# Optimization experiments

Hardware: AMD Instinct MI355X
Metric: run time of the kernel (lower is better)

## Reference

```python
import jax, jax.numpy as jnp
import numpy as np
from jax.ops import segment_sum, segment_max

N, E, IN_DIM, HID, HEADS, B, ACTIONS = 16384, 262144, 512, 256, 4, 64, 32
NEG_SLOPE = 0.2  # PyG GATConv default leaky-relu slope


def setup_inputs() -> dict:
    key = jax.random.key(0)
    ks = jax.random.split(key, 12)
    x = jax.random.normal(ks[0], (N, IN_DIM), dtype=jnp.float32)
    edge_index = jax.random.randint(ks[1], (2, E), 0, N, dtype=jnp.int64)
    batch = jnp.sort(jax.random.randint(ks[2], (N,), 0, B, dtype=jnp.int64))
    s = 0.05
    return {
        "x": x,
        "edge_index": edge_index,
        "batch": batch,
        # SAGEConv: lin_l (neighbors, with bias) + lin_r (root, no bias)
        "sage_w_l": jax.random.normal(ks[3], (IN_DIM, HID), dtype=jnp.float32) * s,
        "sage_b_l": jnp.zeros((HID,), dtype=jnp.float32),
        "sage_w_r": jax.random.normal(ks[4], (IN_DIM, HID), dtype=jnp.float32) * s,
        # GATConv: shared lin, per-head attention vectors, output bias (concat=False)
        "gat_w": jax.random.normal(ks[5], (HID, HEADS * HID), dtype=jnp.float32) * s,
        "gat_att_src": jax.random.normal(ks[6], (HEADS, HID), dtype=jnp.float32) * s,
        "gat_att_dst": jax.random.normal(ks[7], (HEADS, HID), dtype=jnp.float32) * s,
        "gat_b": jnp.zeros((HID,), dtype=jnp.float32),
        # action head
        "head_w": jax.random.normal(ks[8], (HID, ACTIONS), dtype=jnp.float32) * s,
        "head_b": jnp.zeros((ACTIONS,), dtype=jnp.float32),
    }


def reference(x, edge_index, batch, sage_w_l, sage_b_l, sage_w_r,
              gat_w, gat_att_src, gat_att_dst, gat_b, head_w, head_b):
    src, dst = edge_index[0], edge_index[1]

    # ---- SAGEConv (mean aggregation): lin_l(mean_j x_j) + lin_r(x_i) ----
    agg = segment_sum(x[src], dst, num_segments=N)                 # [N, IN_DIM]
    deg = segment_sum(jnp.ones((E,), x.dtype), dst, num_segments=N)
    mean_nbr = agg / jnp.maximum(deg, 1.0)[:, None]
    h = mean_nbr @ sage_w_l + sage_b_l + x @ sage_w_r              # [N, HID]
    h = jax.nn.relu(h)
    # dropout is identity at inference (training=False)

    # ---- GATConv (adds self-loops, concat=False -> head average) ----
    loop = jnp.arange(N, dtype=src.dtype)
    si = jnp.concatenate([src, loop])                              # [E2]
    di = jnp.concatenate([dst, loop])
    g = (h @ gat_w).reshape(N, HEADS, HID)                         # [N, H, C]
    a_src = jnp.einsum('nhc,hc->nh', g, gat_att_src)               # [N, H]
    a_dst = jnp.einsum('nhc,hc->nh', g, gat_att_dst)
    logits = jax.nn.leaky_relu(a_src[si] + a_dst[di], NEG_SLOPE)   # [E2, H]
    m = segment_max(logits, di, num_segments=N)                    # per-target max
    ex = jnp.exp(logits - m[di])
    denom = segment_sum(ex, di, num_segments=N)
    alpha = ex / denom[di]                                         # [E2, H]
    out = segment_sum(g[si] * alpha[:, :, None], di, num_segments=N)  # [N, H, C]
    out = jax.nn.relu(out.mean(axis=1) + gat_b)                    # [N, HID]

    # ---- global mean pool + action head ----
    pooled = segment_sum(out, batch, num_segments=B)
    cnt = segment_sum(jnp.ones((N,), out.dtype), batch, num_segments=B)
    pooled = pooled / jnp.maximum(cnt, 1.0)[:, None]               # [B, HID]
    return pooled @ head_w + head_b                                # [B, ACTIONS]
```

## Files before the change

kernel.cpp:

```cpp
#include <hip/hip_runtime.h>
#include <math.h>

#define N_NODES 16384
#define N_EDGES 262144
#define IN_DIM  512
#define HID     256
#define HEADS   4
#define NBATCH  64
#define ACTIONS 32
#define NEG_SLOPE 0.2f

typedef __attribute__((ext_vector_type(8))) short short8;
typedef __attribute__((ext_vector_type(4))) float f32x4;

__device__ __forceinline__ float lrelu(float v) { return v > 0.f ? v : NEG_SLOPE * v; }

__device__ __forceinline__ unsigned short bf16_rne(float f) {
    union { float f; unsigned int u; } x; x.f = f;
    unsigned int u = x.u;
    unsigned int r = (u + 0x7FFFu + ((u >> 16) & 1u)) >> 16;
    return (unsigned short)r;
}

__device__ __forceinline__ float bf16_to_f32(unsigned short s) {
    union { unsigned int u; float f; } x; x.u = (unsigned int)s << 16;
    return x.f;
}

__device__ __forceinline__ float4 bf4_to_f4(ushort4 u) {
    return make_float4(bf16_to_f32(u.x), bf16_to_f32(u.y), bf16_to_f32(u.z), bf16_to_f32(u.w));
}

__device__ __forceinline__ void async_copy16(const unsigned short* g, unsigned short* l) {
    __builtin_amdgcn_global_load_lds(
        (const __attribute__((address_space(1))) unsigned int*)g,
        (__attribute__((address_space(3))) unsigned int*)l, 16, 0, 0);
}

#define NB_WLR  1024
#define NB_WSTK 1024
#define NB_WATT 8
#define NB_ZERO 128
#define NB_SETUP (NB_WLR + NB_WSTK + NB_WATT + NB_ZERO)

__global__ __launch_bounds__(256) void setup_kernel(
        const float* __restrict__ wl, const float* __restrict__ wr, unsigned short* __restrict__ bt1,
        const float* __restrict__ gat_w, unsigned short* __restrict__ bt2,
        const float* __restrict__ att_src, const float* __restrict__ att_dst, float* __restrict__ watt,
        int* __restrict__ deg, float* __restrict__ pooled) {
    int bid = blockIdx.x, tid = threadIdx.x;
    if (bid < NB_WLR) {
        int idx = bid * 256 + tid;
        int j = idx >> 9;
        int k = idx & 511;
        float v = (j < HID) ? wl[k * HID + j] : wr[k * HID + (j - HID)];
        bt1[idx] = bf16_rne(v);
    } else if (bid < NB_WLR + NB_WSTK) {
        int idx = (bid - NB_WLR) * 256 + tid;
        int c = idx >> 10;
        int r = idx & 1023;
        int h = r >> 8;
        int k = r & 255;
        bt2[idx] = bf16_rne(gat_w[(size_t)k * (HEADS * HID) + h * HID + c]);
    } else if (bid < NB_WLR + NB_WSTK + NB_WATT) {
        int j = bid - NB_WLR - NB_WSTK;
        int c = tid;
        int hh = j & 3;
        const float* att = (j < 4) ? (att_src + hh * HID) : (att_dst + hh * HID);
        float s = 0.f;
        for (int cc = 0; cc < HID; cc++)
            s += gat_w[(size_t)c * (HEADS * HID) + hh * HID + cc] * att[cc];
        watt[j * HID + c] = s;
    } else {
        int idx = (bid - NB_WLR - NB_WSTK - NB_WATT) * 256 + tid;
        if (idx < N_NODES) deg[idx] = 0;
        else pooled[idx - N_NODES] = 0.f;
    }
}

__global__ void deg_kernel(const int* __restrict__ ei, int* __restrict__ deg) {
    int e = blockIdx.x * 256 + threadIdx.x;
    if (e < N_EDGES) atomicAdd(&deg[ei[N_EDGES + e]], 1);
}

__global__ __launch_bounds__(256) void scan_kernel(const int* __restrict__ deg,
                                                   int* __restrict__ row_start,
                                                   int* __restrict__ pos) {
    int t = threadIdx.x;
    int lane = t & 63, wv = t >> 6;
    int base = t * 64;
    int4 buf[16];
    int sum = 0;
#pragma unroll
    for (int i = 0; i < 16; i++) {
        buf[i] = ((const int4*)(deg + base))[i];
        sum += buf[i].x + buf[i].y + buf[i].z + buf[i].w;
    }
    int v = sum;
#pragma unroll
    for (int off = 1; off < 64; off <<= 1) {
        int u = __shfl_up(v, off);
        if (lane >= off) v += u;
    }
    __shared__ int wsum[4];
    if (lane == 63) wsum[wv] = v;
    __syncthreads();
    int wbase = 0;
    for (int w0 = 0; w0 < wv; w0++) wbase += wsum[w0];
    int run = wbase + v - sum;
#pragma unroll
    for (int i = 0; i < 16; i++) {
        int4 b = buf[i];
        int4 o;
        o.x = run; run += b.x;
        o.y = run; run += b.y;
        o.z = run; run += b.z;
        o.w = run; run += b.w;
        ((int4*)(row_start + base))[i] = o;
        ((int4*)(pos + base))[i] = o;
    }
    if (t == 255) row_start[N_NODES] = run;
}

__global__ void fill_kernel(const int* __restrict__ ei, int* __restrict__ pos,
                            int* __restrict__ col) {
    int e = blockIdx.x * 256 + threadIdx.x;
    if (e < N_EDGES) {
        int s = ei[e];
        int d = ei[N_EDGES + e];
        int p = atomicAdd(&pos[d], 1);
        col[p] = s;
    }
}

#define BK 32

__global__ __launch_bounds__(256) void gemm1_kernel(const float* __restrict__ X,
                                                    const unsigned short* __restrict__ Bt,
                                                    unsigned short* __restrict__ Cb,
                                                    int Nn, int K) {
    __shared__ __align__(16) unsigned short As[2][64 * BK];
    __shared__ __align__(16) unsigned short Bs[2][128 * BK];

    int tid  = threadIdx.x;
    int wv   = tid >> 6;
    int lane = tid & 63;
    int m0 = blockIdx.y * 64;
    int n0 = blockIdx.x * 128;
    int wm = (wv & 1) * 32;
    int wn = (wv >> 1) * 64;

    int srow = tid >> 2;
    int scol = (tid & 3) * 8;
    const float*          Xg  = X  + (size_t)(m0 + srow) * K + scol;
    const unsigned short* Bg0 = Bt + (size_t)(n0 + srow) * K + scol;
    const unsigned short* Bg1 = Bt + (size_t)(n0 + 64 + srow) * K + scol;

    int fr = lane & 15;
    int fk = (lane >> 4) * 8;
    f32x4 acc[2][4] = {};

    for (int kt = 0; kt < K; kt += 2 * BK) {
#pragma unroll
        for (int s = 0; s < 2; s++) {
            int ko = kt + s * BK;
            async_copy16(Bg0 + ko, &Bs[s][wv * 512]);
            async_copy16(Bg1 + ko, &Bs[s][2048 + wv * 512]);
            float4 a0 = *(const float4*)(Xg + ko);
            float4 a1 = *(const float4*)(Xg + ko + 4);
            short8 p;
            p[0] = (short)bf16_rne(a0.x); p[1] = (short)bf16_rne(a0.y);
            p[2] = (short)bf16_rne(a0.z); p[3] = (short)bf16_rne(a0.w);
            p[4] = (short)bf16_rne(a1.x); p[5] = (short)bf16_rne(a1.y);
            p[6] = (short)bf16_rne(a1.z); p[7] = (short)bf16_rne(a1.w);
            *(short8*)&As[s][srow * BK + scol] = p;
        }
        __syncthreads();

#pragma unroll
        for (int s = 0; s < 2; s++) {
            short8 af[2], bf[4];
#pragma unroll
            for (int mi = 0; mi < 2; mi++)
                af[mi] = *(const short8*)&As[s][(wm + mi * 16 + fr) * BK + fk];
#pragma unroll
            for (int ni = 0; ni < 4; ni++)
                bf[ni] = *(const short8*)&Bs[s][(wn + ni * 16 + fr) * BK + fk];
#pragma unroll
            for (int mi = 0; mi < 2; mi++)
#pragma unroll
                for (int ni = 0; ni < 4; ni++)
                    acc[mi][ni] = __builtin_amdgcn_mfma_f32_16x16x32_bf16(af[mi], bf[ni], acc[mi][ni], 0, 0, 0);
        }
        __syncthreads();
    }

    int cr = (lane >> 4) * 4;
    int cc = lane & 15;
#pragma unroll
    for (int mi = 0; mi < 2; mi++) {
#pragma unroll
        for (int ni = 0; ni < 4; ni++) {
            int gc = n0 + wn + ni * 16 + cc;
#pragma unroll
            for (int r = 0; r < 4; r++) {
                int gr = m0 + wm + mi * 16 + cr + r;
                Cb[(size_t)gr * Nn + gc] = bf16_rne(acc[mi][ni][r]);
            }
        }
    }
}

__global__ __launch_bounds__(256) void gemm2_pool_kernel(const unsigned short* __restrict__ A,
                                                         const unsigned short* __restrict__ Bt,
                                                         const int* __restrict__ batch,
                                                         const float* __restrict__ bias,
                                                         float scale,
                                                         float* __restrict__ pooled,
                                                         int Nn, int K) {
    __shared__ __align__(16) unsigned short As[2][64 * BK];
    __shared__ __align__(16) unsigned short Bs[2][64 * BK];
    __shared__ int bsh[64];

    int tid  = threadIdx.x;
    int wv   = tid >> 6;
    int lane = tid & 63;
    int m0 = blockIdx.y * 64;
    int n0 = blockIdx.x * 64;
    int wm = (wv & 1) * 32;
    int wn = (wv >> 1) * 32;

    if (tid < 64) bsh[tid] = batch[m0 + tid];

    int srow = tid >> 2;
    int scol = (tid & 3) * 8;
    const unsigned short* Ag = A  + (size_t)(m0 + srow) * K + scol;
    const unsigned short* Bg = Bt + (size_t)(n0 + srow) * K + scol;

    int fr = lane & 15;
    int fk = (lane >> 4) * 8;
    f32x4 acc[2][2] = {};

    for (int kt = 0; kt < K; kt += 2 * BK) {
#pragma unroll
        for (int s = 0; s < 2; s++) {
            int ko = kt + s * BK;
            async_copy16(Ag + ko, &As[s][wv * 512]);
            async_copy16(Bg + ko, &Bs[s][wv * 512]);
        }
        __syncthreads();

#pragma unroll
        for (int s = 0; s < 2; s++) {
            short8 af[2], bf[2];
#pragma unroll
            for (int mi = 0; mi < 2; mi++)
                af[mi] = *(const short8*)&As[s][(wm + mi * 16 + fr) * BK + fk];
#pragma unroll
            for (int ni = 0; ni < 2; ni++)
                bf[ni] = *(const short8*)&Bs[s][(wn + ni * 16 + fr) * BK + fk];
#pragma unroll
            for (int mi = 0; mi < 2; mi++)
#pragma unroll
                for (int ni = 0; ni < 2; ni++)
                    acc[mi][ni] = __builtin_amdgcn_mfma_f32_16x16x32_bf16(af[mi], bf[ni], acc[mi][ni], 0, 0, 0);
        }
        __syncthreads();
    }

    int cr = (lane >> 4) * 4;
    int cc = lane & 15;
#pragma unroll
    for (int mi = 0; mi < 2; mi++) {
        int rowb = wm + mi * 16 + cr;
        int b0 = bsh[rowb], b3 = bsh[rowb + 3];
#pragma unroll
        for (int ni = 0; ni < 2; ni++) {
            int gc = n0 + wn + ni * 16 + cc;
            float b = bias[gc];
            float v0 = fmaxf(fmaf(acc[mi][ni][0], scale, b), 0.f);
            float v1 = fmaxf(fmaf(acc[mi][ni][1], scale, b), 0.f);
            float v2 = fmaxf(fmaf(acc[mi][ni][2], scale, b), 0.f);
            float v3 = fmaxf(fmaf(acc[mi][ni][3], scale, b), 0.f);
            if (b0 == b3) {
                atomicAdd(&pooled[b0 * HID + gc], (v0 + v1) + (v2 + v3));
            } else {
                atomicAdd(&pooled[bsh[rowb + 0] * HID + gc], v0);
                atomicAdd(&pooled[bsh[rowb + 1] * HID + gc], v1);
                atomicAdd(&pooled[bsh[rowb + 2] * HID + gc], v2);
                atomicAdd(&pooled[bsh[rowb + 3] * HID + gc], v3);
            }
        }
    }
}

__global__ __launch_bounds__(256) void sage_agg_kernel(const unsigned short* __restrict__ xlr,
                                                       const int* __restrict__ row_start,
                                                       const int* __restrict__ col,
                                                       const float* __restrict__ b_l,
                                                       const float* __restrict__ watt,
                                                       unsigned short* __restrict__ hb,
                                                       float* __restrict__ a_att) {
    __shared__ float watt_s[8 * HID];
    for (int i = threadIdx.x; i < 8 * HID; i += 256) watt_s[i] = watt[i];
    __syncthreads();

    int wave = threadIdx.x >> 6;
    int lane = threadIdx.x & 63;
    int n = blockIdx.x * 4 + wave;
    int start = row_start[n], end = row_start[n + 1];
    int c0 = lane * 4;

    float4 acc = make_float4(0.f, 0.f, 0.f, 0.f);
    int e = start;
    for (; e + 4 <= end; e += 4) {
        int s0 = col[e], s1 = col[e + 1], s2 = col[e + 2], s3 = col[e + 3];
        ushort4 u0 = *(const ushort4*)(xlr + (size_t)s0 * IN_DIM + c0);
        ushort4 u1 = *(const ushort4*)(xlr + (size_t)s1 * IN_DIM + c0);
        ushort4 u2 = *(const ushort4*)(xlr + (size_t)s2 * IN_DIM + c0);
        ushort4 u3 = *(const ushort4*)(xlr + (size_t)s3 * IN_DIM + c0);
        float4 v0 = bf4_to_f4(u0), v1 = bf4_to_f4(u1), v2 = bf4_to_f4(u2), v3 = bf4_to_f4(u3);
        acc.x += (v0.x + v1.x) + (v2.x + v3.x);
        acc.y += (v0.y + v1.y) + (v2.y + v3.y);
        acc.z += (v0.z + v1.z) + (v2.z + v3.z);
        acc.w += (v0.w + v1.w) + (v2.w + v3.w);
    }
    for (; e < end; e++) {
        int s = col[e];
        float4 v = bf4_to_f4(*(const ushort4*)(xlr + (size_t)s * IN_DIM + c0));
        acc.x += v.x; acc.y += v.y; acc.z += v.z; acc.w += v.w;
    }
    float inv = 1.f / (float)max(end - start, 1);
    float4 xr = bf4_to_f4(*(const ushort4*)(xlr + (size_t)n * IN_DIM + HID + c0));
    float4 bl = *(const float4*)(b_l + c0);
    float4 hv;
    hv.x = fmaxf(fmaf(acc.x, inv, bl.x + xr.x), 0.f);
    hv.y = fmaxf(fmaf(acc.y, inv, bl.y + xr.y), 0.f);
    hv.z = fmaxf(fmaf(acc.z, inv, bl.z + xr.z), 0.f);
    hv.w = fmaxf(fmaf(acc.w, inv, bl.w + xr.w), 0.f);
    ushort4 ho;
    ho.x = bf16_rne(hv.x); ho.y = bf16_rne(hv.y); ho.z = bf16_rne(hv.z); ho.w = bf16_rne(hv.w);
    *(ushort4*)(hb + (size_t)n * HID + c0) = ho;

    float p[8];
#pragma unroll
    for (int j = 0; j < 8; j++) {
        float4 wt = *(const float4*)&watt_s[j * HID + c0];
        p[j] = hv.x * wt.x + hv.y * wt.y + hv.z * wt.z + hv.w * wt.w;
    }
#pragma unroll
    for (int off = 32; off; off >>= 1)
#pragma unroll
        for (int j = 0; j < 8; j++) p[j] += __shfl_down(p[j], off);
    if (lane == 0) {
#pragma unroll
        for (int j = 0; j < 8; j++) a_att[n * 8 + j] = p[j];
    }
}

__global__ __launch_bounds__(256) void gat_agg_kernel(const unsigned short* __restrict__ hb,
                                                      const float* __restrict__ a_att,
                                                      const int* __restrict__ row_start,
                                                      const int* __restrict__ col,
                                                      unsigned short* __restrict__ T) {
    __shared__ __align__(16) float w_s[4][64 * 4];
    int wave = threadIdx.x >> 6;
    int lane = threadIdx.x & 63;
    int n = blockIdx.x * 4 + wave;
    int start = row_start[n], end = row_start[n + 1];

    float4 an = *(const float4*)(a_att + n * 8);
    float4 ad = *(const float4*)(a_att + n * 8 + 4);
    float adst[4] = {ad.x, ad.y, ad.z, ad.w};
    float selfl[4] = {lrelu(an.x + ad.x), lrelu(an.y + ad.y), lrelu(an.z + ad.z), lrelu(an.w + ad.w)};
    float m[4], wself[4];
#pragma unroll
    for (int hh = 0; hh < 4; hh++) {
        m[hh] = fmaxf(selfl[hh], 0.f);
        wself[hh] = __expf(selfl[hh] - m[hh]);
    }

    int c0 = lane * 4;
    float4 hn = bf4_to_f4(*(const ushort4*)(hb + (size_t)n * HID + c0));
    float4 acc[4];
#pragma unroll
    for (int hh = 0; hh < 4; hh++)
        acc[hh] = make_float4(wself[hh] * hn.x, wself[hh] * hn.y, wself[hh] * hn.z, wself[hh] * hn.w);

    float dpart[4] = {0.f, 0.f, 0.f, 0.f};

    for (int base = start; base < end; base += 64) {
        int cnt = min(64, end - base);
        if (lane < cnt) {
            int s = col[base + lane];
            float4 as = *(const float4*)(a_att + s * 8);
            float4 wv;
            wv.x = __expf(lrelu(as.x + adst[0]) - m[0]);
            wv.y = __expf(lrelu(as.y + adst[1]) - m[1]);
            wv.z = __expf(lrelu(as.z + adst[2]) - m[2]);
            wv.w = __expf(lrelu(as.w + adst[3]) - m[3]);
            *(float4*)&w_s[wave][lane * 4] = wv;
            dpart[0] += wv.x; dpart[1] += wv.y; dpart[2] += wv.z; dpart[3] += wv.w;
        }
        __builtin_amdgcn_wave_barrier();

        int i = 0;
        for (; i + 2 <= cnt; i += 2) {
            int s0 = col[base + i], s1 = col[base + i + 1];
            float4 w0 = *(const float4*)&w_s[wave][i * 4];
            float4 w1 = *(const float4*)&w_s[wave][(i + 1) * 4];
            ushort4 u0 = *(const ushort4*)(hb + (size_t)s0 * HID + c0);
            ushort4 u1 = *(const ushort4*)(hb + (size_t)s1 * HID + c0);
            float4 h0 = bf4_to_f4(u0), h1 = bf4_to_f4(u1);
            float wr0[4] = {w0.x, w0.y, w0.z, w0.w};
            float wr1[4] = {w1.x, w1.y, w1.z, w1.w};
#pragma unroll
            for (int hh = 0; hh < 4; hh++) {
                acc[hh].x = fmaf(wr0[hh], h0.x, fmaf(wr1[hh], h1.x, acc[hh].x));
                acc[hh].y = fmaf(wr0[hh], h0.y, fmaf(wr1[hh], h1.y, acc[hh].y));
                acc[hh].z = fmaf(wr0[hh], h0.z, fmaf(wr1[hh], h1.z, acc[hh].z));
                acc[hh].w = fmaf(wr0[hh], h0.w, fmaf(wr1[hh], h1.w, acc[hh].w));
            }
        }
        if (i < cnt) {
            int s0 = col[base + i];
            float4 w0 = *(const float4*)&w_s[wave][i * 4];
            float4 h0 = bf4_to_f4(*(const ushort4*)(hb + (size_t)s0 * HID + c0));
            float wr0[4] = {w0.x, w0.y, w0.z, w0.w};
#pragma unroll
            for (int hh = 0; hh < 4; hh++) {
                acc[hh].x = fmaf(wr0[hh], h0.x, acc[hh].x);
                acc[hh].y = fmaf(wr0[hh], h0.y, acc[hh].y);
                acc[hh].z = fmaf(wr0[hh], h0.z, acc[hh].z);
                acc[hh].w = fmaf(wr0[hh], h0.w, acc[hh].w);
            }
        }
        __builtin_amdgcn_wave_barrier();
    }

#pragma unroll
    for (int off = 32; off; off >>= 1)
#pragma unroll
        for (int hh = 0; hh < 4; hh++) dpart[hh] += __shfl_down(dpart[hh], off);
    float invd[4];
#pragma unroll
    for (int hh = 0; hh < 4; hh++)
        invd[hh] = 1.f / (__shfl(dpart[hh], 0) + wself[hh]);

#pragma unroll
    for (int hh = 0; hh < 4; hh++) {
        ushort4 o;
        o.x = bf16_rne(acc[hh].x * invd[hh]); o.y = bf16_rne(acc[hh].y * invd[hh]);
        o.z = bf16_rne(acc[hh].z * invd[hh]); o.w = bf16_rne(acc[hh].w * invd[hh]);
        *(ushort4*)(T + (size_t)n * (HEADS * HID) + hh * HID + c0) = o;
    }
}

__device__ __forceinline__ int lower_bound_i(const int* a, int n, int v) {
    int lo = 0, hi = n;
    while (lo < hi) {
        int mid = (lo + hi) >> 1;
        if (a[mid] < v) lo = mid + 1; else hi = mid;
    }
    return lo;
}

__global__ __launch_bounds__(256) void head_kernel(const float* __restrict__ pooled,
                                                   const int* __restrict__ batch,
                                                   const float* __restrict__ head_w,
                                                   const float* __restrict__ head_b,
                                                   float* __restrict__ out) {
    __shared__ float sm[HID];
    int b = blockIdx.x;
    int c = threadIdx.x;
    int lo = lower_bound_i(batch, N_NODES, b);
    int hi = lower_bound_i(batch, N_NODES, b + 1);
    int cnt = hi - lo;
    sm[c] = pooled[b * HID + c] / (float)max(cnt, 1);
    __syncthreads();
    if (c < ACTIONS) {
        float acc = head_b[c];
        for (int k = 0; k < HID; k++) acc = fmaf(sm[k], head_w[k * ACTIONS + c], acc);
        out[b * ACTIONS + c] = acc;
    }
}

extern "C" void kernel_launch(void* const* d_in, const int* in_sizes, int n_in,
                              void* d_out, int out_size, void* d_ws, size_t ws_size,
                              hipStream_t stream) {
    const float* x        = (const float*)d_in[0];
    const int*   ei       = (const int*)d_in[1];
    const int*   batch    = (const int*)d_in[2];
    const float* sage_w_l = (const float*)d_in[3];
    const float* sage_b_l = (const float*)d_in[4];
    const float* sage_w_r = (const float*)d_in[5];
    const float* gat_w    = (const float*)d_in[6];
    const float* att_src  = (const float*)d_in[7];
    const float* att_dst  = (const float*)d_in[8];
    const float* gat_b    = (const float*)d_in[9];
    const float* head_w   = (const float*)d_in[10];
    const float* head_b   = (const float*)d_in[11];
    float* out = (float*)d_out;

    char* w = (char*)d_ws;
    float* a_att  = (float*)w; w += (size_t)N_NODES * 8 * 4;
    float* watt   = (float*)w; w += (size_t)8 * HID * 4;
    float* pooled = (float*)w; w += (size_t)NBATCH * HID * 4;
    unsigned short* xlr = (unsigned short*)w; w += (size_t)N_NODES * IN_DIM * 2;
    unsigned short* hb  = (unsigned short*)w; w += (size_t)N_NODES * HID * 2;
    unsigned short* T   = (unsigned short*)w; w += (size_t)N_NODES * HEADS * HID * 2;
    unsigned short* bt1 = (unsigned short*)w; w += (size_t)(2 * HID) * IN_DIM * 2;
    unsigned short* bt2 = (unsigned short*)w; w += (size_t)HID * (HEADS * HID) * 2;
    int* deg      = (int*)w;   w += (size_t)N_NODES * 4;
    int* row_start= (int*)w;   w += (size_t)(N_NODES + 64) * 4;
    int* pos      = (int*)w;   w += (size_t)N_NODES * 4;
    int* col      = (int*)w;   w += (size_t)N_EDGES * 4;

    setup_kernel<<<NB_SETUP, 256, 0, stream>>>(sage_w_l, sage_w_r, bt1,
                                               gat_w, bt2, att_src, att_dst, watt,
                                               deg, pooled);

    deg_kernel<<<N_EDGES / 256, 256, 0, stream>>>(ei, deg);
    scan_kernel<<<1, 256, 0, stream>>>(deg, row_start, pos);
    fill_kernel<<<N_EDGES / 256, 256, 0, stream>>>(ei, pos, col);

    gemm1_kernel<<<dim3((2 * HID) / 128, N_NODES / 64), 256, 0, stream>>>(
        x, bt1, xlr, 2 * HID, IN_DIM);

    sage_agg_kernel<<<N_NODES / 4, 256, 0, stream>>>(xlr, row_start, col, sage_b_l, watt, hb, a_att);

    gat_agg_kernel<<<N_NODES / 4, 256, 0, stream>>>(hb, a_att, row_start, col, T);

    gemm2_pool_kernel<<<dim3(HID / 64, N_NODES / 64), 256, 0, stream>>>(
        T, bt2, batch, gat_b, 0.25f, pooled, HID, HEADS * HID);

    head_kernel<<<NBATCH, 256, 0, stream>>>(pooled, batch, head_w, head_b, out);
}
```

Baseline: 260.3 us.

## Fuse degree and CSR-fill into other kernels, split aggregation into column-half passes

```diff
diff --git a/kernel.cpp b/kernel.cpp
--- a/kernel.cpp
+++ b/kernel.cpp
@@ -27,8 +27,14 @@
     return x.f;
 }
 
-__device__ __forceinline__ float4 bf4_to_f4(ushort4 u) {
-    return make_float4(bf16_to_f32(u.x), bf16_to_f32(u.y), bf16_to_f32(u.z), bf16_to_f32(u.w));
+__device__ __forceinline__ float blo(unsigned int u) {
+    union { unsigned int u; float f; } x; x.u = u << 16; return x.f;
+}
+__device__ __forceinline__ float bhi(unsigned int u) {
+    union { unsigned int u; float f; } x; x.u = u & 0xFFFF0000u; return x.f;
+}
+__device__ __forceinline__ unsigned int pack_bf16x2(float a, float b) {
+    return (unsigned int)bf16_rne(a) | ((unsigned int)bf16_rne(b) << 16);
 }
 
 __device__ __forceinline__ void async_copy16(const unsigned short* g, unsigned short* l) {
@@ -40,14 +46,14 @@
 #define NB_WLR  1024
 #define NB_WSTK 1024
 #define NB_WATT 8
-#define NB_ZERO 128
-#define NB_SETUP (NB_WLR + NB_WSTK + NB_WATT + NB_ZERO)
+#define NB_DEG  1024
+#define NB_SETUP (NB_WLR + NB_WSTK + NB_WATT + NB_DEG)
 
 __global__ __launch_bounds__(256) void setup_kernel(
         const float* __restrict__ wl, const float* __restrict__ wr, unsigned short* __restrict__ bt1,
         const float* __restrict__ gat_w, unsigned short* __restrict__ bt2,
         const float* __restrict__ att_src, const float* __restrict__ att_dst, float* __restrict__ watt,
-        int* __restrict__ deg, float* __restrict__ pooled) {
+        const int* __restrict__ ei, int* __restrict__ deg) {
     int bid = blockIdx.x, tid = threadIdx.x;
     if (bid < NB_WLR) {
         int idx = bid * 256 + tid;
@@ -72,15 +78,9 @@
             s += gat_w[(size_t)c * (HEADS * HID) + hh * HID + cc] * att[cc];
         watt[j * HID + c] = s;
     } else {
-        int idx = (bid - NB_WLR - NB_WSTK - NB_WATT) * 256 + tid;
-        if (idx < N_NODES) deg[idx] = 0;
-        else pooled[idx - N_NODES] = 0.f;
-    }
-}
-
-__global__ void deg_kernel(const int* __restrict__ ei, int* __restrict__ deg) {
-    int e = blockIdx.x * 256 + threadIdx.x;
-    if (e < N_EDGES) atomicAdd(&deg[ei[N_EDGES + e]], 1);
+        int e = (bid - NB_WLR - NB_WSTK - NB_WATT) * 256 + tid;
+        if (e < N_EDGES) atomicAdd(&deg[ei[N_EDGES + e]], 1);
+    }
 }
 
 __global__ __launch_bounds__(256) void scan_kernel(const int* __restrict__ deg,
@@ -122,30 +122,35 @@
     if (t == 255) row_start[N_NODES] = run;
 }
 
-__global__ void fill_kernel(const int* __restrict__ ei, int* __restrict__ pos,
-                            int* __restrict__ col) {
-    int e = blockIdx.x * 256 + threadIdx.x;
-    if (e < N_EDGES) {
-        int s = ei[e];
-        int d = ei[N_EDGES + e];
-        int p = atomicAdd(&pos[d], 1);
-        col[p] = s;
-    }
-}
-
 #define BK 32
 
-__global__ __launch_bounds__(256) void gemm1_kernel(const float* __restrict__ X,
-                                                    const unsigned short* __restrict__ Bt,
-                                                    unsigned short* __restrict__ Cb,
-                                                    int Nn, int K) {
+__global__ __launch_bounds__(256) void gemm1_fill_kernel(const float* __restrict__ X,
+                                                         const unsigned short* __restrict__ Bt,
+                                                         unsigned short* __restrict__ Cb,
+                                                         const int* __restrict__ ei,
+                                                         int* __restrict__ pos,
+                                                         int* __restrict__ col,
+                                                         int Nn, int K) {
     __shared__ __align__(16) unsigned short As[2][64 * BK];
     __shared__ __align__(16) unsigned short Bs[2][128 * BK];
 
     int tid  = threadIdx.x;
+
+    if (blockIdx.y & 1) {
+        int fid = (blockIdx.y >> 1) * 4 + blockIdx.x;
+        int e = fid * 256 + tid;
+        if (e < N_EDGES) {
+            int s = ei[e];
+            int d = ei[N_EDGES + e];
+            int p = atomicAdd(&pos[d], 1);
+            col[p] = s;
+        }
+        return;
+    }
+
     int wv   = tid >> 6;
     int lane = tid & 63;
-    int m0 = blockIdx.y * 64;
+    int m0 = (blockIdx.y >> 1) * 64;
     int n0 = blockIdx.x * 128;
     int wm = (wv & 1) * 32;
     int wn = (wv >> 1) * 64;
@@ -208,6 +213,178 @@
                 Cb[(size_t)gr * Nn + gc] = bf16_rne(acc[mi][ni][r]);
             }
         }
+    }
+}
+
+__global__ __launch_bounds__(256) void sage_pass_kernel(const unsigned short* __restrict__ xlr,
+                                                        const int* __restrict__ row_start,
+                                                        const int* __restrict__ col,
+                                                        const float* __restrict__ b_l,
+                                                        const float* __restrict__ watt,
+                                                        unsigned short* __restrict__ hb,
+                                                        float* __restrict__ a_att) {
+    __shared__ float watt_s[8 * 128];
+    int p = blockIdx.y;
+    for (int i = threadIdx.x; i < 8 * 128; i += 256) {
+        int j = i >> 7, cc = i & 127;
+        watt_s[i] = watt[j * HID + p * 128 + cc];
+    }
+    __syncthreads();
+
+    int wave = threadIdx.x >> 6;
+    int lane = threadIdx.x & 63;
+    int n = blockIdx.x * 4 + wave;
+    int start = row_start[n], end = row_start[n + 1];
+    int lc = lane * 2;
+    int cb = p * 128 + lc;
+    const unsigned short* xg = xlr + cb;
+
+    float ax = 0.f, ay = 0.f;
+    int e = start;
+    for (; e + 4 <= end; e += 4) {
+        int s0 = col[e], s1 = col[e + 1], s2 = col[e + 2], s3 = col[e + 3];
+        unsigned int u0 = *(const unsigned int*)(xg + (size_t)s0 * IN_DIM);
+        unsigned int u1 = *(const unsigned int*)(xg + (size_t)s1 * IN_DIM);
+        unsigned int u2 = *(const unsigned int*)(xg + (size_t)s2 * IN_DIM);
+        unsigned int u3 = *(const unsigned int*)(xg + (size_t)s3 * IN_DIM);
+        ax += (blo(u0) + blo(u1)) + (blo(u2) + blo(u3));
+        ay += (bhi(u0) + bhi(u1)) + (bhi(u2) + bhi(u3));
+    }
+    for (; e < end; e++) {
+        unsigned int u = *(const unsigned int*)(xg + (size_t)col[e] * IN_DIM);
+        ax += blo(u); ay += bhi(u);
+    }
+
+    float inv = 1.f / (float)max(end - start, 1);
+    unsigned int ur = *(const unsigned int*)(xlr + (size_t)n * IN_DIM + HID + cb);
+    float hx = fmaxf(fmaf(ax, inv, b_l[cb] + blo(ur)), 0.f);
+    float hy = fmaxf(fmaf(ay, inv, b_l[cb + 1] + bhi(ur)), 0.f);
+    *(unsigned int*)(hb + (size_t)n * HID + cb) = pack_bf16x2(hx, hy);
+
+    float pj[8];
+#pragma unroll
+    for (int j = 0; j < 8; j++)
+        pj[j] = hx * watt_s[j * 128 + lc] + hy * watt_s[j * 128 + lc + 1];
+#pragma unroll
+    for (int off = 32; off; off >>= 1)
+#pragma unroll
+        for (int j = 0; j < 8; j++) pj[j] += __shfl_down(pj[j], off);
+    if (lane == 0) {
+#pragma unroll
+        for (int j = 0; j < 8; j++) atomicAdd(&a_att[n * 8 + j], pj[j]);
+    }
+}
+
+__global__ __launch_bounds__(256) void gat_w_kernel(const float* __restrict__ a_att,
+                                                    const int* __restrict__ row_start,
+                                                    const int* __restrict__ col,
+                                                    float* __restrict__ ew,
+                                                    float* __restrict__ inv_att) {
+    int wave = threadIdx.x >> 6;
+    int lane = threadIdx.x & 63;
+    int n = blockIdx.x * 4 + wave;
+    int start = row_start[n], end = row_start[n + 1];
+
+    float4 an = *(const float4*)(a_att + n * 8);
+    float4 ad = *(const float4*)(a_att + n * 8 + 4);
+    float sl0 = lrelu(an.x + ad.x), sl1 = lrelu(an.y + ad.y);
+    float sl2 = lrelu(an.z + ad.z), sl3 = lrelu(an.w + ad.w);
+    float m0 = fmaxf(sl0, 0.f), m1 = fmaxf(sl1, 0.f);
+    float m2 = fmaxf(sl2, 0.f), m3 = fmaxf(sl3, 0.f);
+    float w0 = __expf(sl0 - m0), w1 = __expf(sl1 - m1);
+    float w2 = __expf(sl2 - m2), w3 = __expf(sl3 - m3);
+
+    float d0 = 0.f, d1 = 0.f, d2 = 0.f, d3 = 0.f;
+    for (int base = start; base < end; base += 64) {
+        int cnt = min(64, end - base);
+        if (lane < cnt) {
+            int s = col[base + lane];
+            float4 as = *(const float4*)(a_att + s * 8);
+            float4 we;
+            we.x = __expf(lrelu(as.x + ad.x) - m0);
+            we.y = __expf(lrelu(as.y + ad.y) - m1);
+            we.z = __expf(lrelu(as.z + ad.z) - m2);
+            we.w = __expf(lrelu(as.w + ad.w) - m3);
+            *(float4*)(ew + (size_t)(base + lane) * 4) = we;
+            d0 += we.x; d1 += we.y; d2 += we.z; d3 += we.w;
+        }
+    }
+#pragma unroll
+    for (int off = 32; off; off >>= 1) {
+        d0 += __shfl_down(d0, off); d1 += __shfl_down(d1, off);
+        d2 += __shfl_down(d2, off); d3 += __shfl_down(d3, off);
+    }
+    if (lane == 0) {
+        *(float4*)(inv_att + n * 8) = make_float4(w0, w1, w2, w3);
+        *(float4*)(inv_att + n * 8 + 4) =
+            make_float4(1.f / (w0 + d0), 1.f / (w1 + d1), 1.f / (w2 + d2), 1.f / (w3 + d3));
+    }
+}
+
+__global__ __launch_bounds__(256) void gat_pass_kernel(const unsigned short* __restrict__ hb,
+                                                       const float* __restrict__ ew,
+                                                       const float* __restrict__ inv_att,
+                                                       const int* __restrict__ row_start,
+                                                       const int* __restrict__ col,
+                                                       unsigned short* __restrict__ T) {
+    int p = blockIdx.y;
+    int wave = threadIdx.x >> 6;
+    int lane = threadIdx.x & 63;
+    int n = blockIdx.x * 4 + wave;
+    int start = row_start[n], end = row_start[n + 1];
+    int cb = p * 128 + lane * 2;
+    const unsigned short* hg = hb + cb;
+
+    float4 wsf = *(const float4*)(inv_att + n * 8);
+    float4 ivf = *(const float4*)(inv_att + n * 8 + 4);
+    unsigned int un = *(const unsigned int*)(hg + (size_t)n * HID);
+    float hnx = blo(un), hny = bhi(un);
+    float ax[4], ay[4];
+    ax[0] = wsf.x * hnx; ay[0] = wsf.x * hny;
+    ax[1] = wsf.y * hnx; ay[1] = wsf.y * hny;
+    ax[2] = wsf.z * hnx; ay[2] = wsf.z * hny;
+    ax[3] = wsf.w * hnx; ay[3] = wsf.w * hny;
+
+    int e = start;
+    for (; e + 4 <= end; e += 4) {
+        int s0 = col[e], s1 = col[e + 1], s2 = col[e + 2], s3 = col[e + 3];
+        float4 w0 = *(const float4*)(ew + (size_t)e * 4);
+        float4 w1 = *(const float4*)(ew + (size_t)(e + 1) * 4);
+        float4 w2 = *(const float4*)(ew + (size_t)(e + 2) * 4);
+        float4 w3 = *(const float4*)(ew + (size_t)(e + 3) * 4);
+        unsigned int u0 = *(const unsigned int*)(hg + (size_t)s0 * HID);
+        unsigned int u1 = *(const unsigned int*)(hg + (size_t)s1 * HID);
+        unsigned int u2 = *(const unsigned int*)(hg + (size_t)s2 * HID);
+        unsigned int u3 = *(const unsigned int*)(hg + (size_t)s3 * HID);
+        float h0x = blo(u0), h0y = bhi(u0);
+        float h1x = blo(u1), h1y = bhi(u1);
+        float h2x = blo(u2), h2y = bhi(u2);
+        float h3x = blo(u3), h3y = bhi(u3);
+        ax[0] = fmaf(w0.x, h0x, fmaf(w1.x, h1x, fmaf(w2.x, h2x, fmaf(w3.x, h3x, ax[0]))));
+        ay[0] = fmaf(w0.x, h0y, fmaf(w1.x, h1y, fmaf(w2.x, h2y, fmaf(w3.x, h3y, ay[0]))));
+        ax[1] = fmaf(w0.y, h0x, fmaf(w1.y, h1x, fmaf(w2.y, h2x, fmaf(w3.y, h3x, ax[1]))));
+        ay[1] = fmaf(w0.y, h0y, fmaf(w1.y, h1y, fmaf(w2.y, h2y, fmaf(w3.y, h3y, ay[1]))));
+        ax[2] = fmaf(w0.z, h0x, fmaf(w1.z, h1x, fmaf(w2.z, h2x, fmaf(w3.z, h3x, ax[2]))));
+        ay[2] = fmaf(w0.z, h0y, fmaf(w1.z, h1y, fmaf(w2.z, h2y, fmaf(w3.z, h3y, ay[2]))));
+        ax[3] = fmaf(w0.w, h0x, fmaf(w1.w, h1x, fmaf(w2.w, h2x, fmaf(w3.w, h3x, ax[3]))));
+        ay[3] = fmaf(w0.w, h0y, fmaf(w1.w, h1y, fmaf(w2.w, h2y, fmaf(w3.w, h3y, ay[3]))));
+    }
+    for (; e < end; e++) {
+        int s = col[e];
+        float4 w = *(const float4*)(ew + (size_t)e * 4);
+        unsigned int u = *(const unsigned int*)(hg + (size_t)s * HID);
+        float hx = blo(u), hy = bhi(u);
+        ax[0] = fmaf(w.x, hx, ax[0]); ay[0] = fmaf(w.x, hy, ay[0]);
+        ax[1] = fmaf(w.y, hx, ax[1]); ay[1] = fmaf(w.y, hy, ay[1]);
+        ax[2] = fmaf(w.z, hx, ax[2]); ay[2] = fmaf(w.z, hy, ay[2]);
+        ax[3] = fmaf(w.w, hx, ax[3]); ay[3] = fmaf(w.w, hy, ay[3]);
+    }
+
+    float iv[4] = {ivf.x, ivf.y, ivf.z, ivf.w};
+#pragma unroll
+    for (int h = 0; h < 4; h++) {
+        *(unsigned int*)(T + (size_t)n * (HEADS * HID) + h * HID + cb) =
+            pack_bf16x2(ax[h] * iv[h], ay[h] * iv[h]);
     }
 }
 
@@ -291,168 +468,6 @@
                 atomicAdd(&pooled[bsh[rowb + 3] * HID + gc], v3);
             }
         }
-    }
-}
-
-__global__ __launch_bounds__(256) void sage_agg_kernel(const unsigned short* __restrict__ xlr,
-                                                       const int* __restrict__ row_start,
-                                                       const int* __restrict__ col,
-                                                       const float* __restrict__ b_l,
-                                                       const float* __restrict__ watt,
-                                                       unsigned short* __restrict__ hb,
-                                                       float* __restrict__ a_att) {
-    __shared__ float watt_s[8 * HID];
-    for (int i = threadIdx.x; i < 8 * HID; i += 256) watt_s[i] = watt[i];
-    __syncthreads();
-
-    int wave = threadIdx.x >> 6;
-    int lane = threadIdx.x & 63;
-    int n = blockIdx.x * 4 + wave;
-    int start = row_start[n], end = row_start[n + 1];
-    int c0 = lane * 4;
-
-    float4 acc = make_float4(0.f, 0.f, 0.f, 0.f);
-    int e = start;
-    for (; e + 4 <= end; e += 4) {
-        int s0 = col[e], s1 = col[e + 1], s2 = col[e + 2], s3 = col[e + 3];
-        ushort4 u0 = *(const ushort4*)(xlr + (size_t)s0 * IN_DIM + c0);
-        ushort4 u1 = *(const ushort4*)(xlr + (size_t)s1 * IN_DIM + c0);
-        ushort4 u2 = *(const ushort4*)(xlr + (size_t)s2 * IN_DIM + c0);
-        ushort4 u3 = *(const ushort4*)(xlr + (size_t)s3 * IN_DIM + c0);
-        float4 v0 = bf4_to_f4(u0), v1 = bf4_to_f4(u1), v2 = bf4_to_f4(u2), v3 = bf4_to_f4(u3);
-        acc.x += (v0.x + v1.x) + (v2.x + v3.x);
-        acc.y += (v0.y + v1.y) + (v2.y + v3.y);
-        acc.z += (v0.z + v1.z) + (v2.z + v3.z);
-        acc.w += (v0.w + v1.w) + (v2.w + v3.w);
-    }
-    for (; e < end; e++) {
-        int s = col[e];
-        float4 v = bf4_to_f4(*(const ushort4*)(xlr + (size_t)s * IN_DIM + c0));
-        acc.x += v.x; acc.y += v.y; acc.z += v.z; acc.w += v.w;
-    }
-    float inv = 1.f / (float)max(end - start, 1);
-    float4 xr = bf4_to_f4(*(const ushort4*)(xlr + (size_t)n * IN_DIM + HID + c0));
-    float4 bl = *(const float4*)(b_l + c0);
-    float4 hv;
-    hv.x = fmaxf(fmaf(acc.x, inv, bl.x + xr.x), 0.f);
-    hv.y = fmaxf(fmaf(acc.y, inv, bl.y + xr.y), 0.f);
-    hv.z = fmaxf(fmaf(acc.z, inv, bl.z + xr.z), 0.f);
-    hv.w = fmaxf(fmaf(acc.w, inv, bl.w + xr.w), 0.f);
-    ushort4 ho;
-    ho.x = bf16_rne(hv.x); ho.y = bf16_rne(hv.y); ho.z = bf16_rne(hv.z); ho.w = bf16_rne(hv.w);
-    *(ushort4*)(hb + (size_t)n * HID + c0) = ho;
-
-    float p[8];
-#pragma unroll
-    for (int j = 0; j < 8; j++) {
-        float4 wt = *(const float4*)&watt_s[j * HID + c0];
-        p[j] = hv.x * wt.x + hv.y * wt.y + hv.z * wt.z + hv.w * wt.w;
-    }
-#pragma unroll
-    for (int off = 32; off; off >>= 1)
-#pragma unroll
-        for (int j = 0; j < 8; j++) p[j] += __shfl_down(p[j], off);
-    if (lane == 0) {
-#pragma unroll
-        for (int j = 0; j < 8; j++) a_att[n * 8 + j] = p[j];
-    }
-}
-
-__global__ __launch_bounds__(256) void gat_agg_kernel(const unsigned short* __restrict__ hb,
-                                                      const float* __restrict__ a_att,
-                                                      const int* __restrict__ row_start,
-                                                      const int* __restrict__ col,
-                                                      unsigned short* __restrict__ T) {
-    __shared__ __align__(16) float w_s[4][64 * 4];
-    int wave = threadIdx.x >> 6;
-    int lane = threadIdx.x & 63;
-    int n = blockIdx.x * 4 + wave;
-    int start = row_start[n], end = row_start[n + 1];
-
-    float4 an = *(const float4*)(a_att + n * 8);
-    float4 ad = *(const float4*)(a_att + n * 8 + 4);
-    float adst[4] = {ad.x, ad.y, ad.z, ad.w};
-    float selfl[4] = {lrelu(an.x + ad.x), lrelu(an.y + ad.y), lrelu(an.z + ad.z), lrelu(an.w + ad.w)};
-    float m[4], wself[4];
-#pragma unroll
-    for (int hh = 0; hh < 4; hh++) {
-        m[hh] = fmaxf(selfl[hh], 0.f);
-        wself[hh] = __expf(selfl[hh] - m[hh]);
-    }
-
-    int c0 = lane * 4;
-    float4 hn = bf4_to_f4(*(const ushort4*)(hb + (size_t)n * HID + c0));
-    float4 acc[4];
-#pragma unroll
-    for (int hh = 0; hh < 4; hh++)
-        acc[hh] = make_float4(wself[hh] * hn.x, wself[hh] * hn.y, wself[hh] * hn.z, wself[hh] * hn.w);
-
-    float dpart[4] = {0.f, 0.f, 0.f, 0.f};
-
-    for (int base = start; base < end; base += 64) {
-        int cnt = min(64, end - base);
-        if (lane < cnt) {
-            int s = col[base + lane];
-            float4 as = *(const float4*)(a_att + s * 8);
-            float4 wv;
-            wv.x = __expf(lrelu(as.x + adst[0]) - m[0]);
-            wv.y = __expf(lrelu(as.y + adst[1]) - m[1]);
-            wv.z = __expf(lrelu(as.z + adst[2]) - m[2]);
-            wv.w = __expf(lrelu(as.w + adst[3]) - m[3]);
-            *(float4*)&w_s[wave][lane * 4] = wv;
-            dpart[0] += wv.x; dpart[1] += wv.y; dpart[2] += wv.z; dpart[3] += wv.w;
-        }
-        __builtin_amdgcn_wave_barrier();
-
-        int i = 0;
-        for (; i + 2 <= cnt; i += 2) {
-            int s0 = col[base + i], s1 = col[base + i + 1];
-            float4 w0 = *(const float4*)&w_s[wave][i * 4];
-            float4 w1 = *(const float4*)&w_s[wave][(i + 1) * 4];
-            ushort4 u0 = *(const ushort4*)(hb + (size_t)s0 * HID + c0);
-            ushort4 u1 = *(const ushort4*)(hb + (size_t)s1 * HID + c0);
-            float4 h0 = bf4_to_f4(u0), h1 = bf4_to_f4(u1);
-            float wr0[4] = {w0.x, w0.y, w0.z, w0.w};
-            float wr1[4] = {w1.x, w1.y, w1.z, w1.w};
-#pragma unroll
-            for (int hh = 0; hh < 4; hh++) {
-                acc[hh].x = fmaf(wr0[hh], h0.x, fmaf(wr1[hh], h1.x, acc[hh].x));
-                acc[hh].y = fmaf(wr0[hh], h0.y, fmaf(wr1[hh], h1.y, acc[hh].y));
-                acc[hh].z = fmaf(wr0[hh], h0.z, fmaf(wr1[hh], h1.z, acc[hh].z));
-                acc[hh].w = fmaf(wr0[hh], h0.w, fmaf(wr1[hh], h1.w, acc[hh].w));
-            }
-        }
-        if (i < cnt) {
-            int s0 = col[base + i];
-            float4 w0 = *(const float4*)&w_s[wave][i * 4];
-            float4 h0 = bf4_to_f4(*(const ushort4*)(hb + (size_t)s0 * HID + c0));
-            float wr0[4] = {w0.x, w0.y, w0.z, w0.w};
-#pragma unroll
-            for (int hh = 0; hh < 4; hh++) {
-                acc[hh].x = fmaf(wr0[hh], h0.x, acc[hh].x);
-                acc[hh].y = fmaf(wr0[hh], h0.y, acc[hh].y);
-                acc[hh].z = fmaf(wr0[hh], h0.z, acc[hh].z);
-                acc[hh].w = fmaf(wr0[hh], h0.w, acc[hh].w);
-            }
-        }
-        __builtin_amdgcn_wave_barrier();
-    }
-
-#pragma unroll
-    for (int off = 32; off; off >>= 1)
-#pragma unroll
-        for (int hh = 0; hh < 4; hh++) dpart[hh] += __shfl_down(dpart[hh], off);
-    float invd[4];
-#pragma unroll
-    for (int hh = 0; hh < 4; hh++)
-        invd[hh] = 1.f / (__shfl(dpart[hh], 0) + wself[hh]);
-
-#pragma unroll
-    for (int hh = 0; hh < 4; hh++) {
-        ushort4 o;
-        o.x = bf16_rne(acc[hh].x * invd[hh]); o.y = bf16_rne(acc[hh].y * invd[hh]);
-        o.z = bf16_rne(acc[hh].z * invd[hh]); o.w = bf16_rne(acc[hh].w * invd[hh]);
-        *(ushort4*)(T + (size_t)n * (HEADS * HID) + hh * HID + c0) = o;
     }
 }
 
@@ -503,33 +518,40 @@
     float* out = (float*)d_out;
 
     char* w = (char*)d_ws;
+    int*   deg    = (int*)w;   w += (size_t)N_NODES * 4;
     float* a_att  = (float*)w; w += (size_t)N_NODES * 8 * 4;
+    float* pooled = (float*)w; w += (size_t)NBATCH * HID * 4;
+    size_t zero_bytes = (size_t)N_NODES * 4 + (size_t)N_NODES * 8 * 4 + (size_t)NBATCH * HID * 4;
     float* watt   = (float*)w; w += (size_t)8 * HID * 4;
-    float* pooled = (float*)w; w += (size_t)NBATCH * HID * 4;
     unsigned short* xlr = (unsigned short*)w; w += (size_t)N_NODES * IN_DIM * 2;
     unsigned short* hb  = (unsigned short*)w; w += (size_t)N_NODES * HID * 2;
     unsigned short* T   = (unsigned short*)w; w += (size_t)N_NODES * HEADS * HID * 2;
     unsigned short* bt1 = (unsigned short*)w; w += (size_t)(2 * HID) * IN_DIM * 2;
     unsigned short* bt2 = (unsigned short*)w; w += (size_t)HID * (HEADS * HID) * 2;
-    int* deg      = (int*)w;   w += (size_t)N_NODES * 4;
     int* row_start= (int*)w;   w += (size_t)(N_NODES + 64) * 4;
     int* pos      = (int*)w;   w += (size_t)N_NODES * 4;
     int* col      = (int*)w;   w += (size_t)N_EDGES * 4;
+    float* ew     = (float*)w; w += (size_t)N_EDGES * 4 * 4;
+    float* inv_att= (float*)w; w += (size_t)N_NODES * 8 * 4;
+
+    hipMemsetAsync(d_ws, 0, zero_bytes, stream);
 
     setup_kernel<<<NB_SETUP, 256, 0, stream>>>(sage_w_l, sage_w_r, bt1,
                                                gat_w, bt2, att_src, att_dst, watt,
-                                               deg, pooled);
-
-    deg_kernel<<<N_EDGES / 256, 256, 0, stream>>>(ei, deg);
+                                               ei, deg);
+
     scan_kernel<<<1, 256, 0, stream>>>(deg, row_start, pos);
-    fill_kernel<<<N_EDGES / 256, 256, 0, stream>>>(ei, pos, col);
-
-    gemm1_kernel<<<dim3((2 * HID) / 128, N_NODES / 64), 256, 0, stream>>>(
-        x, bt1, xlr, 2 * HID, IN_DIM);
-
-    sage_agg_kernel<<<N_NODES / 4, 256, 0, stream>>>(xlr, row_start, col, sage_b_l, watt, hb, a_att);
-
-    gat_agg_kernel<<<N_NODES / 4, 256, 0, stream>>>(hb, a_att, row_start, col, T);
+
+    gemm1_fill_kernel<<<dim3((2 * HID) / 128, 512), 256, 0, stream>>>(
+        x, bt1, xlr, ei, pos, col, 2 * HID, IN_DIM);
+
+    sage_pass_kernel<<<dim3(N_NODES / 4, 2), 256, 0, stream>>>(
+        xlr, row_start, col, sage_b_l, watt, hb, a_att);
+
+    gat_w_kernel<<<N_NODES / 4, 256, 0, stream>>>(a_att, row_start, col, ew, inv_att);
+
+    gat_pass_kernel<<<dim3(N_NODES / 4, 2), 256, 0, stream>>>(
+        hb, ew, inv_att, row_start, col, T);
 
     gemm2_pool_kernel<<<dim3(HID / 64, N_NODES / 64), 256, 0, stream>>>(
         T, bt2, batch, gat_b, 0.25f, pooled, HID, HEADS * HID);
```

Result: slower. 286.3 us (+10.0%).

## Double-buffer GEMM K-loop shared memory and fold degree count into setup

Applied to the files above, without the earlier changes.

```diff
diff --git a/kernel.cpp b/kernel.cpp
--- a/kernel.cpp
+++ b/kernel.cpp
@@ -40,14 +40,14 @@
 #define NB_WLR  1024
 #define NB_WSTK 1024
 #define NB_WATT 8
-#define NB_ZERO 128
-#define NB_SETUP (NB_WLR + NB_WSTK + NB_WATT + NB_ZERO)
+#define NB_DEG  1024
+#define NB_SETUP (NB_WLR + NB_WSTK + NB_WATT + NB_DEG)
 
 __global__ __launch_bounds__(256) void setup_kernel(
         const float* __restrict__ wl, const float* __restrict__ wr, unsigned short* __restrict__ bt1,
         const float* __restrict__ gat_w, unsigned short* __restrict__ bt2,
         const float* __restrict__ att_src, const float* __restrict__ att_dst, float* __restrict__ watt,
-        int* __restrict__ deg, float* __restrict__ pooled) {
+        const int* __restrict__ ei, int* __restrict__ deg) {
     int bid = blockIdx.x, tid = threadIdx.x;
     if (bid < NB_WLR) {
         int idx = bid * 256 + tid;
@@ -72,15 +72,9 @@
             s += gat_w[(size_t)c * (HEADS * HID) + hh * HID + cc] * att[cc];
         watt[j * HID + c] = s;
     } else {
-        int idx = (bid - NB_WLR - NB_WSTK - NB_WATT) * 256 + tid;
-        if (idx < N_NODES) deg[idx] = 0;
-        else pooled[idx - N_NODES] = 0.f;
-    }
-}
-
-__global__ void deg_kernel(const int* __restrict__ ei, int* __restrict__ deg) {
-    int e = blockIdx.x * 256 + threadIdx.x;
-    if (e < N_EDGES) atomicAdd(&deg[ei[N_EDGES + e]], 1);
+        int e = (bid - NB_WLR - NB_WSTK - NB_WATT) * 256 + tid;
+        if (e < N_EDGES) atomicAdd(&deg[ei[N_EDGES + e]], 1);
+    }
 }
 
 __global__ __launch_bounds__(256) void scan_kernel(const int* __restrict__ deg,
@@ -139,8 +133,8 @@
                                                     const unsigned short* __restrict__ Bt,
                                                     unsigned short* __restrict__ Cb,
                                                     int Nn, int K) {
-    __shared__ __align__(16) unsigned short As[2][64 * BK];
-    __shared__ __align__(16) unsigned short Bs[2][128 * BK];
+    __shared__ __align__(16) unsigned short As[2][2][64 * BK];
+    __shared__ __align__(16) unsigned short Bs[2][2][128 * BK];
 
     int tid  = threadIdx.x;
     int wv   = tid >> 6;
@@ -159,40 +153,71 @@
     int fr = lane & 15;
     int fk = (lane >> 4) * 8;
     f32x4 acc[2][4] = {};
-
+    float4 pa0[2], pa1[2];
+
+#pragma unroll
+    for (int s = 0; s < 2; s++) {
+        int ko = s * BK;
+        async_copy16(Bg0 + ko, &Bs[0][s][wv * 512]);
+        async_copy16(Bg1 + ko, &Bs[0][s][2048 + wv * 512]);
+        pa0[s] = *(const float4*)(Xg + ko);
+        pa1[s] = *(const float4*)(Xg + ko + 4);
+    }
+#pragma unroll
+    for (int s = 0; s < 2; s++) {
+        short8 p;
+        p[0] = (short)bf16_rne(pa0[s].x); p[1] = (short)bf16_rne(pa0[s].y);
+        p[2] = (short)bf16_rne(pa0[s].z); p[3] = (short)bf16_rne(pa0[s].w);
+        p[4] = (short)bf16_rne(pa1[s].x); p[5] = (short)bf16_rne(pa1[s].y);
+        p[6] = (short)bf16_rne(pa1[s].z); p[7] = (short)bf16_rne(pa1[s].w);
+        *(short8*)&As[0][s][srow * BK + scol] = p;
+    }
+    __syncthreads();
+
+    int cur = 0;
     for (int kt = 0; kt < K; kt += 2 * BK) {
-#pragma unroll
-        for (int s = 0; s < 2; s++) {
-            int ko = kt + s * BK;
-            async_copy16(Bg0 + ko, &Bs[s][wv * 512]);
-            async_copy16(Bg1 + ko, &Bs[s][2048 + wv * 512]);
-            float4 a0 = *(const float4*)(Xg + ko);
-            float4 a1 = *(const float4*)(Xg + ko + 4);
-            short8 p;
-            p[0] = (short)bf16_rne(a0.x); p[1] = (short)bf16_rne(a0.y);
-            p[2] = (short)bf16_rne(a0.z); p[3] = (short)bf16_rne(a0.w);
-            p[4] = (short)bf16_rne(a1.x); p[5] = (short)bf16_rne(a1.y);
-            p[6] = (short)bf16_rne(a1.z); p[7] = (short)bf16_rne(a1.w);
-            *(short8*)&As[s][srow * BK + scol] = p;
-        }
-        __syncthreads();
+        int nxt = kt + 2 * BK;
+        bool pf = nxt < K;
+        if (pf) {
+#pragma unroll
+            for (int s = 0; s < 2; s++) {
+                int ko = nxt + s * BK;
+                async_copy16(Bg0 + ko, &Bs[cur ^ 1][s][wv * 512]);
+                async_copy16(Bg1 + ko, &Bs[cur ^ 1][s][2048 + wv * 512]);
+                pa0[s] = *(const float4*)(Xg + ko);
+                pa1[s] = *(const float4*)(Xg + ko + 4);
+            }
+        }
 
 #pragma unroll
         for (int s = 0; s < 2; s++) {
             short8 af[2], bf[4];
 #pragma unroll
             for (int mi = 0; mi < 2; mi++)
-                af[mi] = *(const short8*)&As[s][(wm + mi * 16 + fr) * BK + fk];
+                af[mi] = *(const short8*)&As[cur][s][(wm + mi * 16 + fr) * BK + fk];
 #pragma unroll
             for (int ni = 0; ni < 4; ni++)
-                bf[ni] = *(const short8*)&Bs[s][(wn + ni * 16 + fr) * BK + fk];
+                bf[ni] = *(const short8*)&Bs[cur][s][(wn + ni * 16 + fr) * BK + fk];
 #pragma unroll
             for (int mi = 0; mi < 2; mi++)
 #pragma unroll
                 for (int ni = 0; ni < 4; ni++)
                     acc[mi][ni] = __builtin_amdgcn_mfma_f32_16x16x32_bf16(af[mi], bf[ni], acc[mi][ni], 0, 0, 0);
         }
+
+        if (pf) {
+#pragma unroll
+            for (int s = 0; s < 2; s++) {
+                short8 p;
+                p[0] = (short)bf16_rne(pa0[s].x); p[1] = (short)bf16_rne(pa0[s].y);
+                p[2] = (short)bf16_rne(pa0[s].z); p[3] = (short)bf16_rne(pa0[s].w);
+                p[4] = (short)bf16_rne(pa1[s].x); p[5] = (short)bf16_rne(pa1[s].y);
+                p[6] = (short)bf16_rne(pa1[s].z); p[7] = (short)bf16_rne(pa1[s].w);
+                *(short8*)&As[cur ^ 1][s][srow * BK + scol] = p;
+            }
+        }
         __syncthreads();
+        cur ^= 1;
     }
 
     int cr = (lane >> 4) * 4;
@@ -218,8 +243,8 @@
                                                          float scale,
                                                          float* __restrict__ pooled,
                                                          int Nn, int K) {
-    __shared__ __align__(16) unsigned short As[2][64 * BK];
-    __shared__ __align__(16) unsigned short Bs[2][64 * BK];
+    __shared__ __align__(16) unsigned short As[2][2][64 * BK];
+    __shared__ __align__(16) unsigned short Bs[2][2][64 * BK];
     __shared__ int bsh[64];
 
     int tid  = threadIdx.x;
@@ -241,24 +266,36 @@
     int fk = (lane >> 4) * 8;
     f32x4 acc[2][2] = {};
 
+#pragma unroll
+    for (int s = 0; s < 2; s++) {
+        int ko = s * BK;
+        async_copy16(Ag + ko, &As[0][s][wv * 512]);
+        async_copy16(Bg + ko, &Bs[0][s][wv * 512]);
+    }
+    __syncthreads();
+
+    int cur = 0;
     for (int kt = 0; kt < K; kt += 2 * BK) {
-#pragma unroll
-        for (int s = 0; s < 2; s++) {
-            int ko = kt + s * BK;
-            async_copy16(Ag + ko, &As[s][wv * 512]);
-            async_copy16(Bg + ko, &Bs[s][wv * 512]);
-        }
-        __syncthreads();
+        int nxt = kt + 2 * BK;
+        bool pf = nxt < K;
+        if (pf) {
+#pragma unroll
+            for (int s = 0; s < 2; s++) {
+                int ko = nxt + s * BK;
+                async_copy16(Ag + ko, &As[cur ^ 1][s][wv * 512]);
+                async_copy16(Bg + ko, &Bs[cur ^ 1][s][wv * 512]);
+            }
+        }
 
 #pragma unroll
         for (int s = 0; s < 2; s++) {
             short8 af[2], bf[2];
 #pragma unroll
             for (int mi = 0; mi < 2; mi++)
-                af[mi] = *(const short8*)&As[s][(wm + mi * 16 + fr) * BK + fk];
+                af[mi] = *(const short8*)&As[cur][s][(wm + mi * 16 + fr) * BK + fk];
 #pragma unroll
             for (int ni = 0; ni < 2; ni++)
-                bf[ni] = *(const short8*)&Bs[s][(wn + ni * 16 + fr) * BK + fk];
+                bf[ni] = *(const short8*)&Bs[cur][s][(wn + ni * 16 + fr) * BK + fk];
 #pragma unroll
             for (int mi = 0; mi < 2; mi++)
 #pragma unroll
@@ -266,6 +303,7 @@
                     acc[mi][ni] = __builtin_amdgcn_mfma_f32_16x16x32_bf16(af[mi], bf[ni], acc[mi][ni], 0, 0, 0);
         }
         __syncthreads();
+        cur ^= 1;
     }
 
     int cr = (lane >> 4) * 4;
@@ -503,24 +541,26 @@
     float* out = (float*)d_out;
 
     char* w = (char*)d_ws;
+    int*   deg    = (int*)w;   w += (size_t)N_NODES * 4;
+    float* pooled = (float*)w; w += (size_t)NBATCH * HID * 4;
+    size_t zero_bytes = (size_t)N_NODES * 4 + (size_t)NBATCH * HID * 4;
     float* a_att  = (float*)w; w += (size_t)N_NODES * 8 * 4;
     float* watt   = (float*)w; w += (size_t)8 * HID * 4;
-    float* pooled = (float*)w; w += (size_t)NBATCH * HID * 4;
     unsigned short* xlr = (unsigned short*)w; w += (size_t)N_NODES * IN_DIM * 2;
     unsigned short* hb  = (unsigned short*)w; w += (size_t)N_NODES * HID * 2;
     unsigned short* T   = (unsigned short*)w; w += (size_t)N_NODES * HEADS * HID * 2;
     unsigned short* bt1 = (unsigned short*)w; w += (size_t)(2 * HID) * IN_DIM * 2;
     unsigned short* bt2 = (unsigned short*)w; w += (size_t)HID * (HEADS * HID) * 2;
-    int* deg      = (int*)w;   w += (size_t)N_NODES * 4;
     int* row_start= (int*)w;   w += (size_t)(N_NODES + 64) * 4;
     int* pos      = (int*)w;   w += (size_t)N_NODES * 4;
     int* col      = (int*)w;   w += (size_t)N_EDGES * 4;
 
+    hipMemsetAsync(d_ws, 0, zero_bytes, stream);
+
     setup_kernel<<<NB_SETUP, 256, 0, stream>>>(sage_w_l, sage_w_r, bt1,
                                                gat_w, bt2, att_src, att_dst, watt,
-                                               deg, pooled);
-
-    deg_kernel<<<N_EDGES / 256, 256, 0, stream>>>(ei, deg);
+                                               ei, deg);
+
     scan_kernel<<<1, 256, 0, stream>>>(deg, row_start, pos);
     fill_kernel<<<N_EDGES / 256, 256, 0, stream>>>(ei, pos, col);
 
```

After: 263.1 us. About the same (+1.0%).
